# Optimization experiments

Hardware: AMD Instinct MI355X
Metric: run time of the kernel (lower is better)

Reference implementation:

```python
import math
import jax, jax.numpy as jnp
import numpy as np

N, K, M, H, D, F = 4, 2048, 512, 8, 64, 2048
EPS = 1e-10


def setup_inputs() -> dict:
    key = jax.random.key(0)
    ks = jax.random.split(key, 8)
    c_qkv = math.sqrt(6 / (M + D))  # matches nn.init.uniform_(-c, c)
    c_p = math.sqrt(6 / (M + D))
    c_ff1 = math.sqrt(6 / (M + F))
    return {
        "x": jax.random.normal(ks[0], (N, K, M), jnp.float32),
        "Wq": jax.random.uniform(ks[1], (H, M, D), jnp.float32, -c_qkv, c_qkv),
        "bq": jnp.zeros((H, D), jnp.float32),
        "Wk": jax.random.uniform(ks[2], (H, M, D), jnp.float32, -c_qkv, c_qkv),
        "bk": jnp.zeros((H, D), jnp.float32),
        "Wv": jax.random.uniform(ks[3], (H, M, D), jnp.float32, -c_qkv, c_qkv),
        "bv": jnp.zeros((H, D), jnp.float32),
        "Wp": jax.random.uniform(ks[4], (H * D, M), jnp.float32, -c_p, c_p),
        "bp": jnp.zeros((M,), jnp.float32),
        "gamma1": jnp.ones((M,), jnp.float32),
        "beta1": jnp.zeros((M,), jnp.float32),
        "W1": jax.random.uniform(ks[5], (M, F), jnp.float32, -c_ff1, c_ff1),
        "b1": jnp.zeros((F,), jnp.float32),
        "W2": jax.random.uniform(ks[6], (F, M), jnp.float32, -c_ff1, c_ff1),
        "b2": jnp.zeros((M,), jnp.float32),
        "gamma2": jnp.ones((M,), jnp.float32),
        "beta2": jnp.zeros((M,), jnp.float32),
    }


def _layer_norm(z, gamma, beta):
    # matches the module: std = sqrt(mean((z-mean)^2)); y = gamma*(z-mean)/(std+eps)+beta
    mean = jnp.mean(z, axis=-1, keepdims=True)
    zc = z - mean
    std = jnp.sqrt(jnp.mean(zc * zc, axis=-1, keepdims=True))
    return gamma * (zc / (std + EPS)) + beta


def reference(x, Wq, bq, Wk, bk, Wv, bv, Wp, bp, gamma1, beta1, W1, b1, W2, b2, gamma2, beta2):
    # multi-head self-attention (query=key=value=x, no mask)
    q = jnp.einsum('nkm,hmd->hnkd', x, Wq) + bq[:, None, None, :]
    k = jnp.einsum('nkm,hmd->hnkd', x, Wk) + bk[:, None, None, :]
    v = jnp.einsum('nkm,hmd->hnkd', x, Wv) + bv[:, None, None, :]
    scale = 1.0 / math.sqrt(D)  # sqrt(dim_q) as in the source (M = query.shape[-1] = dim_q)
    scores = jnp.einsum('hnkd,hnld->hnkl', q, k) * scale  # full K x K matrix per head
    weights = jax.nn.softmax(scores, axis=-1)
    heads = jnp.einsum('hnkl,hnld->hnkd', weights, v)
    concat = heads.transpose(1, 2, 0, 3).reshape(N, K, H * D)
    attn = concat @ Wp + bp
    # residual + LN, FFN, residual + LN (dropout = 0.0 -> identity)
    x1 = _layer_norm(x + attn, gamma1, beta1)
    ff = jax.nn.relu(x1 @ W1 + b1) @ W2 + b2
    return _layer_norm(x1 + ff, gamma2, beta2)
```

## Files before the change

### kernel.cpp

```cpp
#include <hip/hip_runtime.h>
#include <cstdint>
#include <cstddef>

typedef unsigned short u16;
typedef __attribute__((ext_vector_type(8))) __bf16 bf16x8;
typedef __attribute__((ext_vector_type(4))) float f32x4;

#define DEV __device__ __forceinline__


DEV u16 f2bf(float f) {
  union { float f; unsigned u; } a; a.f = f;
  return (u16)((a.u + 0x7fffu + ((a.u >> 16) & 1u)) >> 16);
}

DEV void gld_lds16(const void* g, void* l) {
  __builtin_amdgcn_global_load_lds(
      (__attribute__((address_space(1))) void*)(g),
      (__attribute__((address_space(3))) void*)(l),
      16, 0, 0);
}

__global__ void __launch_bounds__(256) cast_x_kernel(const float* __restrict__ x,
                                                     u16* __restrict__ xb) {
  int i = (blockIdx.x * 256 + threadIdx.x) * 4;
  float4 v = *(const float4*)(x + i);
  u16 o0 = f2bf(v.x), o1 = f2bf(v.y), o2 = f2bf(v.z), o3 = f2bf(v.w);
  ushort4 o; o.x = o0; o.y = o1; o.z = o2; o.w = o3;
  *(ushort4*)(xb + i) = o;
}

__global__ void __launch_bounds__(256) pack_w_kernel(
    const float* __restrict__ Wq, const float* __restrict__ Wk, const float* __restrict__ Wv,
    const float* __restrict__ Wp, const float* __restrict__ W1, const float* __restrict__ W2,
    u16* __restrict__ WqkvT, u16* __restrict__ WpT, u16* __restrict__ W1T, u16* __restrict__ W2T) {
  int i = blockIdx.x * 256 + threadIdx.x;
  if (i < 786432) {
    int c = i >> 9, m = i & 511;
    float v;
    if (c < 512)        v = Wq[((c >> 6) << 15) + (m << 6) + (c & 63)];
    else if (c < 1024) { int c2 = c - 512;  v = Wk[((c2 >> 6) << 15) + (m << 6) + (c2 & 63)]; }
    else               { int c2 = c - 1024; v = Wv[((c2 >> 6) << 15) + (m << 6) + (c2 & 63)]; }
    WqkvT[i] = f2bf(v);
  } else if (i < 786432 + 262144) {
    int j = i - 786432; int n = j >> 9, k = j & 511;
    WpT[j] = f2bf(Wp[(k << 9) + n]);
  } else if (i < 786432 + 262144 + 1048576) {
    int j = i - (786432 + 262144); int f = j >> 9, m = j & 511;
    W1T[j] = f2bf(W1[(m << 11) + f]);
  } else {
    int j = i - (786432 + 262144 + 1048576); int mm = j >> 11, f = j & 2047;
    W2T[j] = f2bf(W2[(f << 9) + mm]);
  }
}

template <int EPI>
__global__ void __launch_bounds__(256, 2) gemm_bf16(
    const u16* __restrict__ A, const u16* __restrict__ BT,
    int Mg, int Ng, int Kg,
    const float* __restrict__ b0, const float* __restrict__ b1, const float* __restrict__ b2,
    const float* __restrict__ resid,
    void* __restrict__ o0, void* __restrict__ o1, void* __restrict__ o2) {
  __shared__ __align__(16) u16 As[128 * 32];
  __shared__ __align__(16) u16 Bs[128 * 32];
  const int tid = threadIdx.x;
  const int w = tid >> 6, l = tid & 63;
  const int lr = l & 15, lg = l >> 4;
  const int tn = Ng >> 7;
  const int bm = blockIdx.x / tn, bn = blockIdx.x % tn;
  const int row0 = bm << 7, col0 = bn << 7;
  const int wm = (w >> 1) << 6, wn = (w & 1) << 6;

  f32x4 acc[4][4];
#pragma unroll
  for (int i = 0; i < 4; i++)
#pragma unroll
    for (int j = 0; j < 4; j++) acc[i][j] = f32x4{0.f, 0.f, 0.f, 0.f};

  const int srow = w * 32 + (l >> 2);
  const int scol = (l & 3) << 3;
  const size_t aBase = (size_t)(row0 + srow) * Kg + scol;
  const size_t bBase = (size_t)(col0 + srow) * Kg + scol;

  const int nk = Kg >> 5;
  for (int kt = 0; kt < nk; ++kt) {
    const int k0 = kt << 5;
    gld_lds16(A + aBase + k0,                      &As[(w * 32) * 32]);
    gld_lds16(A + aBase + k0 + (size_t)16 * Kg,    &As[(w * 32 + 16) * 32]);
    gld_lds16(BT + bBase + k0,                     &Bs[(w * 32) * 32]);
    gld_lds16(BT + bBase + k0 + (size_t)16 * Kg,   &Bs[(w * 32 + 16) * 32]);
    __syncthreads();

    bf16x8 af[4], bfv[4];
#pragma unroll
    for (int mi = 0; mi < 4; mi++)
      af[mi] = *(const bf16x8*)&As[(wm + mi * 16 + lr) * 32 + (lg << 3)];
#pragma unroll
    for (int ni = 0; ni < 4; ni++)
      bfv[ni] = *(const bf16x8*)&Bs[(wn + ni * 16 + lr) * 32 + (lg << 3)];
#pragma unroll
    for (int mi = 0; mi < 4; mi++)
#pragma unroll
      for (int ni = 0; ni < 4; ni++)
        acc[mi][ni] = __builtin_amdgcn_mfma_f32_16x16x32_bf16(af[mi], bfv[ni], acc[mi][ni], 0, 0, 0);
    __syncthreads();
  }

#pragma unroll
  for (int mi = 0; mi < 4; mi++) {
    const int growb = row0 + wm + mi * 16 + lg * 4;
#pragma unroll
    for (int ni = 0; ni < 4; ni++) {
      const int gcol = col0 + wn + ni * 16 + lr;
#pragma unroll
      for (int r = 0; r < 4; r++) {
        const float v = acc[mi][ni][r];
        const int t = growb + r;
        if constexpr (EPI == 0) {
          const int n = t >> 11, ktok = t & 2047;
          if (gcol < 512) {
            const int h = gcol >> 6, d = gcol & 63;
            ((u16*)o0)[((size_t)((h << 2) + n) * 2048 + ktok) * 64 + d] = f2bf(v + b0[gcol]);
          } else if (gcol < 1024) {
            const int c = gcol - 512, h = c >> 6, d = c & 63;
            ((u16*)o1)[((size_t)((h << 2) + n) * 2048 + ktok) * 64 + d] = f2bf(v + b1[c]);
          } else {
            const int c = gcol - 1024, h = c >> 6, d = c & 63;
            ((u16*)o2)[((size_t)((h << 2) + n) * 64 + d) * 2048 + ktok] = f2bf(v + b2[c]);
          }
        } else if constexpr (EPI == 1 || EPI == 3) {
          ((float*)o0)[(size_t)t * Ng + gcol] = v + b0[gcol] + resid[(size_t)t * Ng + gcol];
        } else {
          const float u = v + b0[gcol];
          ((u16*)o0)[(size_t)t * Ng + gcol] = f2bf(u > 0.f ? u : 0.f);
        }
      }
    }
  }
}

__global__ void __launch_bounds__(256, 2) attn_kernel(
    const u16* __restrict__ Q, const u16* __restrict__ K, const u16* __restrict__ Vt,
    u16* __restrict__ attnb) {
  __shared__ __align__(16) u16 Ks[64 * 72];
  __shared__ __align__(16) u16 Vs[64 * 72];
  __shared__ __align__(16) u16 Ps[4][32 * 72];
  const int tid = threadIdx.x, w = tid >> 6, l = tid & 63;
  const int lr = l & 15, lg = l >> 4;
  const int hn = blockIdx.y;
  const int qbase = blockIdx.x * 128 + w * 32;
  const u16* Qhn = Q + (size_t)hn * 2048 * 64;
  const u16* Khn = K + (size_t)hn * 2048 * 64;
  const u16* Vhn = Vt + (size_t)hn * 64 * 2048;

  bf16x8 qf[2][2];
#pragma unroll
  for (int mf = 0; mf < 2; mf++)
#pragma unroll
    for (int kk = 0; kk < 2; kk++)
      qf[mf][kk] = *(const bf16x8*)&Qhn[(size_t)(qbase + mf * 16 + lr) * 64 + kk * 32 + (lg << 3)];

  float mst[2][4], lst[2][4];
  f32x4 oacc[2][4];
#pragma unroll
  for (int mf = 0; mf < 2; mf++) {
#pragma unroll
    for (int r = 0; r < 4; r++) { mst[mf][r] = -1e30f; lst[mf][r] = 0.f; }
#pragma unroll
    for (int df = 0; df < 4; df++) oacc[mf][df] = f32x4{0.f, 0.f, 0.f, 0.f};
  }

  const int strow = tid >> 2;
  const int stcb = (tid & 3) << 4;

  for (int kt = 0; kt < 32; ++kt) {
    const int kv0 = kt << 6;
    {
      const u16* gk = &Khn[(size_t)(kv0 + strow) * 64 + stcb];
      *(uint4*)&Ks[strow * 72 + stcb]     = *(const uint4*)gk;
      *(uint4*)&Ks[strow * 72 + stcb + 8] = *(const uint4*)(gk + 8);
      const u16* gv = &Vhn[(size_t)strow * 2048 + kv0 + stcb];
      *(uint4*)&Vs[strow * 72 + stcb]     = *(const uint4*)gv;
      *(uint4*)&Vs[strow * 72 + stcb + 8] = *(const uint4*)(gv + 8);
    }
    __syncthreads();

    f32x4 s[2][4];
#pragma unroll
    for (int mf = 0; mf < 2; mf++)
#pragma unroll
      for (int nf = 0; nf < 4; nf++) s[mf][nf] = f32x4{0.f, 0.f, 0.f, 0.f};
#pragma unroll
    for (int kk = 0; kk < 2; kk++) {
#pragma unroll
      for (int nf = 0; nf < 4; nf++) {
        bf16x8 kf = *(const bf16x8*)&Ks[(nf * 16 + lr) * 72 + kk * 32 + (lg << 3)];
        s[0][nf] = __builtin_amdgcn_mfma_f32_16x16x32_bf16(qf[0][kk], kf, s[0][nf], 0, 0, 0);
        s[1][nf] = __builtin_amdgcn_mfma_f32_16x16x32_bf16(qf[1][kk], kf, s[1][nf], 0, 0, 0);
      }
    }

#pragma unroll
    for (int mf = 0; mf < 2; mf++) {
      float mnew[4], sc[4], rs[4];
#pragma unroll
      for (int nf = 0; nf < 4; nf++)
#pragma unroll
        for (int r = 0; r < 4; r++) s[mf][nf][r] *= 0.125f;
#pragma unroll
      for (int r = 0; r < 4; r++) {
        float mx = fmaxf(fmaxf(s[mf][0][r], s[mf][1][r]), fmaxf(s[mf][2][r], s[mf][3][r]));
#pragma unroll
        for (int off = 1; off < 16; off <<= 1) mx = fmaxf(mx, __shfl_xor(mx, off));
        mnew[r] = fmaxf(mst[mf][r], mx);
        sc[r] = __expf(mst[mf][r] - mnew[r]);
        mst[mf][r] = mnew[r];
        rs[r] = 0.f;
      }
#pragma unroll
      for (int nf = 0; nf < 4; nf++)
#pragma unroll
        for (int r = 0; r < 4; r++) {
          float p = __expf(s[mf][nf][r] - mnew[r]);
          s[mf][nf][r] = p;
          rs[r] += p;
        }
#pragma unroll
      for (int r = 0; r < 4; r++) {
#pragma unroll
        for (int off = 1; off < 16; off <<= 1) rs[r] += __shfl_xor(rs[r], off);
        lst[mf][r] = lst[mf][r] * sc[r] + rs[r];
      }
#pragma unroll
      for (int df = 0; df < 4; df++)
#pragma unroll
        for (int r = 0; r < 4; r++) oacc[mf][df][r] *= sc[r];
#pragma unroll
      for (int nf = 0; nf < 4; nf++)
#pragma unroll
        for (int r = 0; r < 4; r++)
          Ps[w][(mf * 16 + lg * 4 + r) * 72 + nf * 16 + lr] = f2bf(s[mf][nf][r]);
    }

#pragma unroll
    for (int kk = 0; kk < 2; kk++) {
      bf16x8 p0 = *(const bf16x8*)&Ps[w][(0 + lr) * 72 + kk * 32 + (lg << 3)];
      bf16x8 p1 = *(const bf16x8*)&Ps[w][(16 + lr) * 72 + kk * 32 + (lg << 3)];
#pragma unroll
      for (int df = 0; df < 4; df++) {
        bf16x8 vf = *(const bf16x8*)&Vs[(df * 16 + lr) * 72 + kk * 32 + (lg << 3)];
        oacc[0][df] = __builtin_amdgcn_mfma_f32_16x16x32_bf16(p0, vf, oacc[0][df], 0, 0, 0);
        oacc[1][df] = __builtin_amdgcn_mfma_f32_16x16x32_bf16(p1, vf, oacc[1][df], 0, 0, 0);
      }
    }
    __syncthreads();
  }

  const int h = hn >> 2, n = hn & 3;
#pragma unroll
  for (int mf = 0; mf < 2; mf++)
#pragma unroll
    for (int df = 0; df < 4; df++)
#pragma unroll
      for (int r = 0; r < 4; r++) {
        const int q = qbase + mf * 16 + lg * 4 + r;
        const int c = h * 64 + df * 16 + lr;
        const float v = oacc[mf][df][r] / lst[mf][r];
        attnb[(size_t)(n * 2048 + q) * 512 + c] = f2bf(v);
      }
}

template <int WRITE_B>
__global__ void __launch_bounds__(256) ln_kernel(
    const float* __restrict__ z, const float* __restrict__ gamma, const float* __restrict__ beta,
    float* __restrict__ outf, u16* __restrict__ outb) {
  const int row = blockIdx.x, tid = threadIdx.x;
  const float* zr = z + (size_t)row * 512;
  const float x0 = zr[tid], x1 = zr[tid + 256];
  float s = x0 + x1, ss = x0 * x0 + x1 * x1;
#pragma unroll
  for (int off = 32; off; off >>= 1) { s += __shfl_down(s, off); ss += __shfl_down(ss, off); }
  __shared__ float red[8];
  if ((tid & 63) == 0) { red[tid >> 6] = s; red[4 + (tid >> 6)] = ss; }
  __syncthreads();
  s = red[0] + red[1] + red[2] + red[3];
  ss = red[4] + red[5] + red[6] + red[7];
  const float mean = s * (1.f / 512.f);
  const float var = ss * (1.f / 512.f) - mean * mean;
  const float inv = 1.f / (sqrtf(fmaxf(var, 0.f)) + 1e-10f);
  const float y0 = gamma[tid] * ((x0 - mean) * inv) + beta[tid];
  const float y1 = gamma[tid + 256] * ((x1 - mean) * inv) + beta[tid + 256];
  outf[(size_t)row * 512 + tid] = y0;
  outf[(size_t)row * 512 + tid + 256] = y1;
  if (WRITE_B) {
    outb[(size_t)row * 512 + tid] = f2bf(y0);
    outb[(size_t)row * 512 + tid + 256] = f2bf(y1);
  }
}

extern "C" void kernel_launch(void* const* d_in, const int* in_sizes, int n_in,
                              void* d_out, int out_size, void* d_ws, size_t ws_size,
                              hipStream_t stream) {
  (void)in_sizes; (void)n_in; (void)out_size; (void)ws_size;
  const float* x   = (const float*)d_in[0];
  const float* Wq  = (const float*)d_in[1];
  const float* bq  = (const float*)d_in[2];
  const float* Wk  = (const float*)d_in[3];
  const float* bk  = (const float*)d_in[4];
  const float* Wv  = (const float*)d_in[5];
  const float* bv  = (const float*)d_in[6];
  const float* Wp  = (const float*)d_in[7];
  const float* bp  = (const float*)d_in[8];
  const float* g1  = (const float*)d_in[9];
  const float* be1 = (const float*)d_in[10];
  const float* W1  = (const float*)d_in[11];
  const float* b1  = (const float*)d_in[12];
  const float* W2  = (const float*)d_in[13];
  const float* b2  = (const float*)d_in[14];
  const float* g2  = (const float*)d_in[15];
  const float* be2 = (const float*)d_in[16];
  float* out = (float*)d_out;
  char* ws = (char*)d_ws;

  u16* xb    = (u16*)(ws + 0);
  u16* WqkvT = (u16*)(ws + 8388608);
  u16* Qb    = (u16*)(ws + 9961472);
  u16* Kb    = (u16*)(ws + 18350080);
  u16* Vtb   = (u16*)(ws + 26738688);
  u16* ff1b  = (u16*)(ws + 0);
  u16* attnb = (u16*)(ws + 35127296);
  u16* WpT   = (u16*)(ws + 43515904);
  u16* W1T   = (u16*)(ws + 44040192);
  u16* W2T   = (u16*)(ws + 46137344);
  float* zb  = (float*)(ws + 48234496);
  float* x1f = (float*)(ws + 65011712);
  u16* x1b   = (u16*)(ws + 81788928);

  cast_x_kernel<<<4096, 256, 0, stream>>>(x, xb);
  pack_w_kernel<<<12288, 256, 0, stream>>>(Wq, Wk, Wv, Wp, W1, W2, WqkvT, WpT, W1T, W2T);
  gemm_bf16<0><<<64 * 12, 256, 0, stream>>>(xb, WqkvT, 8192, 1536, 512,
                                            bq, bk, bv, nullptr, Qb, Kb, Vtb);
  attn_kernel<<<dim3(16, 32), 256, 0, stream>>>(Qb, Kb, Vtb, attnb);
  gemm_bf16<1><<<64 * 4, 256, 0, stream>>>(attnb, WpT, 8192, 512, 512,
                                           bp, nullptr, nullptr, x, zb, nullptr, nullptr);
  ln_kernel<1><<<8192, 256, 0, stream>>>(zb, g1, be1, x1f, x1b);
  gemm_bf16<2><<<64 * 16, 256, 0, stream>>>(x1b, W1T, 8192, 2048, 512,
                                            b1, nullptr, nullptr, nullptr, ff1b, nullptr, nullptr);
  gemm_bf16<3><<<64 * 4, 256, 0, stream>>>(ff1b, W2T, 8192, 512, 2048,
                                           b2, nullptr, nullptr, x1f, zb, nullptr, nullptr);
  ln_kernel<0><<<8192, 256, 0, stream>>>(zb, g2, be2, out, nullptr);
}
```

Baseline: 382.7 us.

## Restructure attention kernel with prefetch, swizzled LDS, folded scale; templatize GEMM tiles

The attention kernel now gives each wave 16 query rows instead of 32, which doubles the grid and raises the occupancy hint. K/V tiles are prefetched into registers one iteration ahead, and LDS uses an XOR swizzle in place of padding. The softmax scale and log2(e) are folded into Wq and bq so the kernel can use exp2 with no per-score multiply, and P is rounded to bf16 with a cheaper conversion. MFMA sections are wrapped in s_setprio. The GEMM is templated on tile size, and the two N=512 GEMMs use 64x128 tiles so more blocks fill the device. The trade-off is less reuse of K/V per block and slightly different rounding of P.

```diff
diff --git a/kernel.cpp b/kernel.cpp
--- a/kernel.cpp
+++ b/kernel.cpp
@@ -8,10 +8,15 @@
 
 #define DEV __device__ __forceinline__
 
+#define QSCALE 0.18033688011112042f
 
 DEV u16 f2bf(float f) {
   union { float f; unsigned u; } a; a.f = f;
   return (u16)((a.u + 0x7fffu + ((a.u >> 16) & 1u)) >> 16);
+}
+DEV u16 f2bf_fast(float f) {
+  union { float f; unsigned u; } a; a.f = f;
+  return (u16)((a.u + 0x8000u) >> 16);
 }
 
 DEV void gld_lds16(const void* g, void* l) {
@@ -21,12 +26,13 @@
       16, 0, 0);
 }
 
+DEV int swz(int row, int cb) { return row * 128 + (cb ^ ((row & 7) << 4)); }
+
 __global__ void __launch_bounds__(256) cast_x_kernel(const float* __restrict__ x,
                                                      u16* __restrict__ xb) {
   int i = (blockIdx.x * 256 + threadIdx.x) * 4;
   float4 v = *(const float4*)(x + i);
-  u16 o0 = f2bf(v.x), o1 = f2bf(v.y), o2 = f2bf(v.z), o3 = f2bf(v.w);
-  ushort4 o; o.x = o0; o.y = o1; o.z = o2; o.w = o3;
+  ushort4 o; o.x = f2bf(v.x); o.y = f2bf(v.y); o.z = f2bf(v.z); o.w = f2bf(v.w);
   *(ushort4*)(xb + i) = o;
 }
 
@@ -38,7 +44,7 @@
   if (i < 786432) {
     int c = i >> 9, m = i & 511;
     float v;
-    if (c < 512)        v = Wq[((c >> 6) << 15) + (m << 6) + (c & 63)];
+    if (c < 512)        v = Wq[((c >> 6) << 15) + (m << 6) + (c & 63)] * QSCALE;
     else if (c < 1024) { int c2 = c - 512;  v = Wk[((c2 >> 6) << 15) + (m << 6) + (c2 & 63)]; }
     else               { int c2 = c - 1024; v = Wv[((c2 >> 6) << 15) + (m << 6) + (c2 & 63)]; }
     WqkvT[i] = f2bf(v);
@@ -54,63 +60,65 @@
   }
 }
 
-template <int EPI>
+template <int EPI, int BM, int BN>
 __global__ void __launch_bounds__(256, 2) gemm_bf16(
     const u16* __restrict__ A, const u16* __restrict__ BT,
     int Mg, int Ng, int Kg,
     const float* __restrict__ b0, const float* __restrict__ b1, const float* __restrict__ b2,
     const float* __restrict__ resid,
     void* __restrict__ o0, void* __restrict__ o1, void* __restrict__ o2) {
-  __shared__ __align__(16) u16 As[128 * 32];
-  __shared__ __align__(16) u16 Bs[128 * 32];
+  constexpr int MI = BM / 32, NI = BN / 32;
+  __shared__ __align__(16) u16 As[BM * 32];
+  __shared__ __align__(16) u16 Bs[BN * 32];
   const int tid = threadIdx.x;
   const int w = tid >> 6, l = tid & 63;
   const int lr = l & 15, lg = l >> 4;
-  const int tn = Ng >> 7;
+  const int tn = Ng / BN;
   const int bm = blockIdx.x / tn, bn = blockIdx.x % tn;
-  const int row0 = bm << 7, col0 = bn << 7;
-  const int wm = (w >> 1) << 6, wn = (w & 1) << 6;
-
-  f32x4 acc[4][4];
-#pragma unroll
-  for (int i = 0; i < 4; i++)
-#pragma unroll
-    for (int j = 0; j < 4; j++) acc[i][j] = f32x4{0.f, 0.f, 0.f, 0.f};
-
-  const int srow = w * 32 + (l >> 2);
+  const int row0 = bm * BM, col0 = bn * BN;
+  const int wm = (w >> 1) * (BM / 2), wn = (w & 1) * (BN / 2);
+
+  f32x4 acc[MI][NI];
+#pragma unroll
+  for (int i = 0; i < MI; i++)
+#pragma unroll
+    for (int j = 0; j < NI; j++) acc[i][j] = f32x4{0.f, 0.f, 0.f, 0.f};
+
   const int scol = (l & 3) << 3;
-  const size_t aBase = (size_t)(row0 + srow) * Kg + scol;
-  const size_t bBase = (size_t)(col0 + srow) * Kg + scol;
+  const size_t aBase = (size_t)(row0 + w * (BM / 4) + (l >> 2)) * Kg + scol;
+  const size_t bBase = (size_t)(col0 + w * (BN / 4) + (l >> 2)) * Kg + scol;
 
   const int nk = Kg >> 5;
   for (int kt = 0; kt < nk; ++kt) {
     const int k0 = kt << 5;
-    gld_lds16(A + aBase + k0,                      &As[(w * 32) * 32]);
-    gld_lds16(A + aBase + k0 + (size_t)16 * Kg,    &As[(w * 32 + 16) * 32]);
-    gld_lds16(BT + bBase + k0,                     &Bs[(w * 32) * 32]);
-    gld_lds16(BT + bBase + k0 + (size_t)16 * Kg,   &Bs[(w * 32 + 16) * 32]);
+#pragma unroll
+    for (int i = 0; i < BM / 64; i++)
+      gld_lds16(A + aBase + k0 + (size_t)(i * 16) * Kg, &As[(w * (BM / 4) + i * 16) * 32]);
+#pragma unroll
+    for (int i = 0; i < BN / 64; i++)
+      gld_lds16(BT + bBase + k0 + (size_t)(i * 16) * Kg, &Bs[(w * (BN / 4) + i * 16) * 32]);
     __syncthreads();
 
-    bf16x8 af[4], bfv[4];
-#pragma unroll
-    for (int mi = 0; mi < 4; mi++)
+    bf16x8 af[MI], bfv[NI];
+#pragma unroll
+    for (int mi = 0; mi < MI; mi++)
       af[mi] = *(const bf16x8*)&As[(wm + mi * 16 + lr) * 32 + (lg << 3)];
 #pragma unroll
-    for (int ni = 0; ni < 4; ni++)
+    for (int ni = 0; ni < NI; ni++)
       bfv[ni] = *(const bf16x8*)&Bs[(wn + ni * 16 + lr) * 32 + (lg << 3)];
 #pragma unroll
-    for (int mi = 0; mi < 4; mi++)
-#pragma unroll
-      for (int ni = 0; ni < 4; ni++)
+    for (int mi = 0; mi < MI; mi++)
+#pragma unroll
+      for (int ni = 0; ni < NI; ni++)
         acc[mi][ni] = __builtin_amdgcn_mfma_f32_16x16x32_bf16(af[mi], bfv[ni], acc[mi][ni], 0, 0, 0);
     __syncthreads();
   }
 
 #pragma unroll
-  for (int mi = 0; mi < 4; mi++) {
+  for (int mi = 0; mi < MI; mi++) {
     const int growb = row0 + wm + mi * 16 + lg * 4;
 #pragma unroll
-    for (int ni = 0; ni < 4; ni++) {
+    for (int ni = 0; ni < NI; ni++) {
       const int gcol = col0 + wn + ni * 16 + lr;
 #pragma unroll
       for (int r = 0; r < 4; r++) {
@@ -120,7 +128,7 @@
           const int n = t >> 11, ktok = t & 2047;
           if (gcol < 512) {
             const int h = gcol >> 6, d = gcol & 63;
-            ((u16*)o0)[((size_t)((h << 2) + n) * 2048 + ktok) * 64 + d] = f2bf(v + b0[gcol]);
+            ((u16*)o0)[((size_t)((h << 2) + n) * 2048 + ktok) * 64 + d] = f2bf(v + b0[gcol] * QSCALE);
           } else if (gcol < 1024) {
             const int c = gcol - 512, h = c >> 6, d = c & 63;
             ((u16*)o1)[((size_t)((h << 2) + n) * 2048 + ktok) * 64 + d] = f2bf(v + b1[c]);
@@ -139,135 +147,126 @@
   }
 }
 
-__global__ void __launch_bounds__(256, 2) attn_kernel(
+__global__ void __launch_bounds__(256, 4) attn_kernel(
     const u16* __restrict__ Q, const u16* __restrict__ K, const u16* __restrict__ Vt,
     u16* __restrict__ attnb) {
-  __shared__ __align__(16) u16 Ks[64 * 72];
-  __shared__ __align__(16) u16 Vs[64 * 72];
-  __shared__ __align__(16) u16 Ps[4][32 * 72];
+  __shared__ __align__(16) u16 Ks[64 * 64];
+  __shared__ __align__(16) u16 Vs[64 * 64];
+  __shared__ __align__(16) u16 Ps[4][16 * 64];
   const int tid = threadIdx.x, w = tid >> 6, l = tid & 63;
   const int lr = l & 15, lg = l >> 4;
   const int hn = blockIdx.y;
-  const int qbase = blockIdx.x * 128 + w * 32;
+  const int qbase = blockIdx.x * 64 + w * 16;
   const u16* Qhn = Q + (size_t)hn * 2048 * 64;
   const u16* Khn = K + (size_t)hn * 2048 * 64;
   const u16* Vhn = Vt + (size_t)hn * 64 * 2048;
-
-  bf16x8 qf[2][2];
-#pragma unroll
-  for (int mf = 0; mf < 2; mf++)
+  char* psw = (char*)&Ps[w][0];
+
+  bf16x8 qf[2];
+#pragma unroll
+  for (int kk = 0; kk < 2; kk++)
+    qf[kk] = *(const bf16x8*)&Qhn[(size_t)(qbase + lr) * 64 + kk * 32 + (lg << 3)];
+
+  float mst[4], lst[4];
+  f32x4 oacc[4];
+#pragma unroll
+  for (int r = 0; r < 4; r++) { mst[r] = -1e30f; lst[r] = 0.f; }
+#pragma unroll
+  for (int df = 0; df < 4; df++) oacc[df] = f32x4{0.f, 0.f, 0.f, 0.f};
+
+  const int srow = tid >> 2;
+  const int scol16 = (tid & 3) << 4;
+  const int cb = scol16 << 1;
+  const u16* kPtr = Khn + (size_t)srow * 64 + scol16;
+  const u16* vPtr = Vhn + (size_t)srow * 2048 + scol16;
+
+  uint4 kr0 = *(const uint4*)(kPtr);
+  uint4 kr1 = *(const uint4*)(kPtr + 8);
+  uint4 vr0 = *(const uint4*)(vPtr);
+  uint4 vr1 = *(const uint4*)(vPtr + 8);
+
+  for (int kt = 0; kt < 32; ++kt) {
+    __syncthreads();
+    *(uint4*)((char*)Ks + swz(srow, cb))      = kr0;
+    *(uint4*)((char*)Ks + swz(srow, cb + 16)) = kr1;
+    *(uint4*)((char*)Vs + swz(srow, cb))      = vr0;
+    *(uint4*)((char*)Vs + swz(srow, cb + 16)) = vr1;
+    __syncthreads();
+    if (kt < 31) {
+      const size_t kv1 = (size_t)(kt + 1) << 6;
+      kr0 = *(const uint4*)(kPtr + kv1 * 64);
+      kr1 = *(const uint4*)(kPtr + kv1 * 64 + 8);
+      vr0 = *(const uint4*)(vPtr + kv1);
+      vr1 = *(const uint4*)(vPtr + kv1 + 8);
+    }
+
+    f32x4 s[4];
+#pragma unroll
+    for (int nf = 0; nf < 4; nf++) s[nf] = f32x4{0.f, 0.f, 0.f, 0.f};
+    __builtin_amdgcn_s_setprio(1);
 #pragma unroll
     for (int kk = 0; kk < 2; kk++)
-      qf[mf][kk] = *(const bf16x8*)&Qhn[(size_t)(qbase + mf * 16 + lr) * 64 + kk * 32 + (lg << 3)];
-
-  float mst[2][4], lst[2][4];
-  f32x4 oacc[2][4];
-#pragma unroll
-  for (int mf = 0; mf < 2; mf++) {
-#pragma unroll
-    for (int r = 0; r < 4; r++) { mst[mf][r] = -1e30f; lst[mf][r] = 0.f; }
-#pragma unroll
-    for (int df = 0; df < 4; df++) oacc[mf][df] = f32x4{0.f, 0.f, 0.f, 0.f};
-  }
-
-  const int strow = tid >> 2;
-  const int stcb = (tid & 3) << 4;
-
-  for (int kt = 0; kt < 32; ++kt) {
-    const int kv0 = kt << 6;
-    {
-      const u16* gk = &Khn[(size_t)(kv0 + strow) * 64 + stcb];
-      *(uint4*)&Ks[strow * 72 + stcb]     = *(const uint4*)gk;
-      *(uint4*)&Ks[strow * 72 + stcb + 8] = *(const uint4*)(gk + 8);
-      const u16* gv = &Vhn[(size_t)strow * 2048 + kv0 + stcb];
-      *(uint4*)&Vs[strow * 72 + stcb]     = *(const uint4*)gv;
-      *(uint4*)&Vs[strow * 72 + stcb + 8] = *(const uint4*)(gv + 8);
-    }
-    __syncthreads();
-
-    f32x4 s[2][4];
-#pragma unroll
-    for (int mf = 0; mf < 2; mf++)
-#pragma unroll
-      for (int nf = 0; nf < 4; nf++) s[mf][nf] = f32x4{0.f, 0.f, 0.f, 0.f};
+#pragma unroll
+      for (int nf = 0; nf < 4; nf++) {
+        bf16x8 kf = *(const bf16x8*)((const char*)Ks + swz(nf * 16 + lr, kk * 64 + lg * 16));
+        s[nf] = __builtin_amdgcn_mfma_f32_16x16x32_bf16(qf[kk], kf, s[nf], 0, 0, 0);
+      }
+    __builtin_amdgcn_s_setprio(0);
+
+    float mnew[4], sc[4];
+#pragma unroll
+    for (int r = 0; r < 4; r++) {
+      float mx = fmaxf(fmaxf(s[0][r], s[1][r]), fmaxf(s[2][r], s[3][r]));
+#pragma unroll
+      for (int off = 1; off < 16; off <<= 1) mx = fmaxf(mx, __shfl_xor(mx, off));
+      mnew[r] = fmaxf(mst[r], mx);
+      sc[r] = exp2f(mst[r] - mnew[r]);
+      mst[r] = mnew[r];
+    }
+    float rs[4] = {0.f, 0.f, 0.f, 0.f};
+#pragma unroll
+    for (int nf = 0; nf < 4; nf++)
+#pragma unroll
+      for (int r = 0; r < 4; r++) {
+        float p = exp2f(s[nf][r] - mnew[r]);
+        rs[r] += p;
+        *(u16*)(psw + swz(lg * 4 + r, 2 * (nf * 16 + lr))) = f2bf_fast(p);
+      }
+#pragma unroll
+    for (int r = 0; r < 4; r++) {
+#pragma unroll
+      for (int off = 1; off < 16; off <<= 1) rs[r] += __shfl_xor(rs[r], off);
+      lst[r] = lst[r] * sc[r] + rs[r];
+    }
+#pragma unroll
+    for (int df = 0; df < 4; df++)
+#pragma unroll
+      for (int r = 0; r < 4; r++) oacc[df][r] *= sc[r];
+
+    __builtin_amdgcn_s_setprio(1);
 #pragma unroll
     for (int kk = 0; kk < 2; kk++) {
-#pragma unroll
-      for (int nf = 0; nf < 4; nf++) {
-        bf16x8 kf = *(const bf16x8*)&Ks[(nf * 16 + lr) * 72 + kk * 32 + (lg << 3)];
-        s[0][nf] = __builtin_amdgcn_mfma_f32_16x16x32_bf16(qf[0][kk], kf, s[0][nf], 0, 0, 0);
-        s[1][nf] = __builtin_amdgcn_mfma_f32_16x16x32_bf16(qf[1][kk], kf, s[1][nf], 0, 0, 0);
+      bf16x8 pa = *(const bf16x8*)((const char*)psw + swz(lr, kk * 64 + lg * 16));
+#pragma unroll
+      for (int df = 0; df < 4; df++) {
+        bf16x8 vf = *(const bf16x8*)((const char*)Vs + swz(df * 16 + lr, kk * 64 + lg * 16));
+        oacc[df] = __builtin_amdgcn_mfma_f32_16x16x32_bf16(pa, vf, oacc[df], 0, 0, 0);
       }
     }
-
-#pragma unroll
-    for (int mf = 0; mf < 2; mf++) {
-      float mnew[4], sc[4], rs[4];
-#pragma unroll
-      for (int nf = 0; nf < 4; nf++)
-#pragma unroll
-        for (int r = 0; r < 4; r++) s[mf][nf][r] *= 0.125f;
-#pragma unroll
-      for (int r = 0; r < 4; r++) {
-        float mx = fmaxf(fmaxf(s[mf][0][r], s[mf][1][r]), fmaxf(s[mf][2][r], s[mf][3][r]));
-#pragma unroll
-        for (int off = 1; off < 16; off <<= 1) mx = fmaxf(mx, __shfl_xor(mx, off));
-        mnew[r] = fmaxf(mst[mf][r], mx);
-        sc[r] = __expf(mst[mf][r] - mnew[r]);
-        mst[mf][r] = mnew[r];
-        rs[r] = 0.f;
-      }
-#pragma unroll
-      for (int nf = 0; nf < 4; nf++)
-#pragma unroll
-        for (int r = 0; r < 4; r++) {
-          float p = __expf(s[mf][nf][r] - mnew[r]);
-          s[mf][nf][r] = p;
-          rs[r] += p;
-        }
-#pragma unroll
-      for (int r = 0; r < 4; r++) {
-#pragma unroll
-        for (int off = 1; off < 16; off <<= 1) rs[r] += __shfl_xor(rs[r], off);
-        lst[mf][r] = lst[mf][r] * sc[r] + rs[r];
-      }
-#pragma unroll
-      for (int df = 0; df < 4; df++)
-#pragma unroll
-        for (int r = 0; r < 4; r++) oacc[mf][df][r] *= sc[r];
-#pragma unroll
-      for (int nf = 0; nf < 4; nf++)
-#pragma unroll
-        for (int r = 0; r < 4; r++)
-          Ps[w][(mf * 16 + lg * 4 + r) * 72 + nf * 16 + lr] = f2bf(s[mf][nf][r]);
-    }
-
-#pragma unroll
-    for (int kk = 0; kk < 2; kk++) {
-      bf16x8 p0 = *(const bf16x8*)&Ps[w][(0 + lr) * 72 + kk * 32 + (lg << 3)];
-      bf16x8 p1 = *(const bf16x8*)&Ps[w][(16 + lr) * 72 + kk * 32 + (lg << 3)];
-#pragma unroll
-      for (int df = 0; df < 4; df++) {
-        bf16x8 vf = *(const bf16x8*)&Vs[(df * 16 + lr) * 72 + kk * 32 + (lg << 3)];
-        oacc[0][df] = __builtin_amdgcn_mfma_f32_16x16x32_bf16(p0, vf, oacc[0][df], 0, 0, 0);
-        oacc[1][df] = __builtin_amdgcn_mfma_f32_16x16x32_bf16(p1, vf, oacc[1][df], 0, 0, 0);
-      }
-    }
-    __syncthreads();
+    __builtin_amdgcn_s_setprio(0);
   }
 
   const int h = hn >> 2, n = hn & 3;
 #pragma unroll
-  for (int mf = 0; mf < 2; mf++)
-#pragma unroll
-    for (int df = 0; df < 4; df++)
-#pragma unroll
-      for (int r = 0; r < 4; r++) {
-        const int q = qbase + mf * 16 + lg * 4 + r;
-        const int c = h * 64 + df * 16 + lr;
-        const float v = oacc[mf][df][r] / lst[mf][r];
-        attnb[(size_t)(n * 2048 + q) * 512 + c] = f2bf(v);
-      }
+  for (int r = 0; r < 4; r++) {
+    const int q = qbase + lg * 4 + r;
+    const float inv = 1.f / lst[r];
+#pragma unroll
+    for (int df = 0; df < 4; df++) {
+      const int c = h * 64 + df * 16 + lr;
+      attnb[(size_t)(n * 2048 + q) * 512 + c] = f2bf(oacc[df][r] * inv);
+    }
+  }
 }
 
 template <int WRITE_B>
@@ -338,15 +337,15 @@
 
   cast_x_kernel<<<4096, 256, 0, stream>>>(x, xb);
   pack_w_kernel<<<12288, 256, 0, stream>>>(Wq, Wk, Wv, Wp, W1, W2, WqkvT, WpT, W1T, W2T);
-  gemm_bf16<0><<<64 * 12, 256, 0, stream>>>(xb, WqkvT, 8192, 1536, 512,
-                                            bq, bk, bv, nullptr, Qb, Kb, Vtb);
-  attn_kernel<<<dim3(16, 32), 256, 0, stream>>>(Qb, Kb, Vtb, attnb);
-  gemm_bf16<1><<<64 * 4, 256, 0, stream>>>(attnb, WpT, 8192, 512, 512,
-                                           bp, nullptr, nullptr, x, zb, nullptr, nullptr);
+  gemm_bf16<0, 128, 128><<<768, 256, 0, stream>>>(xb, WqkvT, 8192, 1536, 512,
+                                                  bq, bk, bv, nullptr, Qb, Kb, Vtb);
+  attn_kernel<<<dim3(32, 32), 256, 0, stream>>>(Qb, Kb, Vtb, attnb);
+  gemm_bf16<1, 64, 128><<<512, 256, 0, stream>>>(attnb, WpT, 8192, 512, 512,
+                                                 bp, nullptr, nullptr, x, zb, nullptr, nullptr);
   ln_kernel<1><<<8192, 256, 0, stream>>>(zb, g1, be1, x1f, x1b);
-  gemm_bf16<2><<<64 * 16, 256, 0, stream>>>(x1b, W1T, 8192, 2048, 512,
-                                            b1, nullptr, nullptr, nullptr, ff1b, nullptr, nullptr);
-  gemm_bf16<3><<<64 * 4, 256, 0, stream>>>(ff1b, W2T, 8192, 512, 2048,
-                                           b2, nullptr, nullptr, x1f, zb, nullptr, nullptr);
+  gemm_bf16<2, 128, 128><<<1024, 256, 0, stream>>>(x1b, W1T, 8192, 2048, 512,
+                                                   b1, nullptr, nullptr, nullptr, ff1b, nullptr, nullptr);
+  gemm_bf16<3, 64, 128><<<512, 256, 0, stream>>>(ff1b, W2T, 8192, 512, 2048,
+                                                 b2, nullptr, nullptr, x1f, zb, nullptr, nullptr);
   ln_kernel<0><<<8192, 256, 0, stream>>>(zb, g2, be2, out, nullptr);
 }
```

Measured after the change: 362.6 us. 5.3% less time.
